# Performance work log

Measured on AMD Instinct MI355X. Metric: run time of the kernel, lower is better.

The kernel has to match this reference:

```python
import jax, jax.numpy as jnp
import numpy as np

N = 400_000      # total nodes
H = 256          # hidden_dim
G = 1024         # num_graphs (static; torch derives it from batch_idx.max()+1)
E1, E2, E3 = 7, 70, 300


def _linear_params(key, fan_in, fan_out):
    kw, kb = jax.random.split(key)
    bound = 1.0 / np.sqrt(fan_in)
    w = jax.random.uniform(kw, (fan_in, fan_out), jnp.float32, -bound, bound)
    b = jax.random.uniform(kb, (fan_out,), jnp.float32, -bound, bound)
    return w, b


def setup_inputs() -> dict:
    key = jax.random.key(0)
    ks = jax.random.split(key, 9)
    node_embeddings = jax.random.normal(ks[0], (N, H), jnp.float32)
    batch_idx = jnp.sort(jax.random.randint(ks[1], (N,), 0, G, jnp.int32))
    pool_w, pool_b = _linear_params(ks[2], H, H)
    ec1_w1, ec1_b1 = _linear_params(ks[3], H, H // 2)
    ec1_w2, ec1_b2 = _linear_params(ks[4], H // 2, E1)
    ec2_w1, ec2_b1 = _linear_params(ks[5], H + E1, H // 2)
    ec2_w2, ec2_b2 = _linear_params(ks[6], H // 2, E2)
    ec3_w1, ec3_b1 = _linear_params(ks[7], H + E1 + E2, H // 2)
    ec3_w2, ec3_b2 = _linear_params(ks[8], H // 2, E3)
    return {
        'node_embeddings': node_embeddings, 'batch_idx': batch_idx,
        'pool_w': pool_w, 'pool_b': pool_b,
        'ec1_w1': ec1_w1, 'ec1_b1': ec1_b1, 'ec1_w2': ec1_w2, 'ec1_b2': ec1_b2,
        'ec2_w1': ec2_w1, 'ec2_b1': ec2_b1, 'ec2_w2': ec2_w2, 'ec2_b2': ec2_b2,
        'ec3_w1': ec3_w1, 'ec3_b1': ec3_b1, 'ec3_w2': ec3_w2, 'ec3_b2': ec3_b2,
    }


def reference(node_embeddings, batch_idx,
              pool_w, pool_b,
              ec1_w1, ec1_b1, ec1_w2, ec1_b2,
              ec2_w1, ec2_b1, ec2_w2, ec2_b2,
              ec3_w1, ec3_b1, ec3_w2, ec3_b2):
    # segment mean pooling: replaces the python loop over graphs in torch
    sums = jax.ops.segment_sum(node_embeddings, batch_idx, num_segments=G)
    counts = jax.ops.segment_sum(jnp.ones((node_embeddings.shape[0],), jnp.float32),
                                 batch_idx, num_segments=G)
    global_feat = sums / jnp.maximum(counts, 1.0)[:, None]  # [G, H]

    gelu = lambda x: jax.nn.gelu(x, approximate=False)  # torch GELU default = exact erf
    g = gelu(global_feat @ pool_w + pool_b)  # dropout is identity in eval

    ec1_logits = gelu(g @ ec1_w1 + ec1_b1) @ ec1_w2 + ec1_b2           # [G, E1]
    ec1_probs = jax.nn.softmax(ec1_logits, axis=-1)

    x2 = jnp.concatenate([g, ec1_probs], axis=-1)                      # [G, H+E1]
    ec2_logits = gelu(x2 @ ec2_w1 + ec2_b1) @ ec2_w2 + ec2_b2          # [G, E2]
    ec2_probs = jax.nn.softmax(ec2_logits, axis=-1)

    x3 = jnp.concatenate([g, ec1_probs, ec2_probs], axis=-1)           # [G, H+E1+E2]
    ec3_logits = gelu(x3 @ ec3_w1 + ec3_b1) @ ec3_w2 + ec3_b2          # [G, E3]

    return (ec1_logits, ec2_logits, ec3_logits, ec1_probs, g)
```

## Files before the change

kernel.cpp:

```cpp
#include <hip/hip_runtime.h>
#include <hip/hip_bf16.h>
#include <math.h>

#define NN 400000
#define GG 1024
#define E1 7
#define E2 70
#define E3 300

#define OFF_L1 0
#define OFF_L2 7168
#define OFF_L3 78848
#define OFF_P1 386048
#define OFF_G  393216

typedef float f32x4 __attribute__((ext_vector_type(4)));

__device__ __forceinline__ float gelu_exact(float v) {
  return 0.5f * v * (1.0f + erff(v * 0.70710678118654752f));
}

__global__ __launch_bounds__(256) void fused_kernel(
    const float* __restrict__ emb, const int* __restrict__ bidx,
    const float* __restrict__ pool_w, const float* __restrict__ pool_b,
    const float* __restrict__ w11, const float* __restrict__ b11,
    const float* __restrict__ w12, const float* __restrict__ b12,
    const float* __restrict__ w21, const float* __restrict__ b21,
    const float* __restrict__ w22, const float* __restrict__ b22,
    const float* __restrict__ w31, const float* __restrict__ b31,
    const float* __restrict__ w32, const float* __restrict__ b32,
    float* __restrict__ out) {
  const int g0 = blockIdx.x * 2;
  const int tid = threadIdx.x;
  const int wave = tid >> 6, lane = tid & 63;

  __shared__ int seg[3];
  __shared__ float xs[2][336];
  __shared__ float hs[2][128];
  __shared__ float os[2][72];
  __shared__ f32x4 red[4][64];

  if (tid < 3) {
    const int target = g0 + tid;
    int lo = 0, hi = NN;
    while (lo < hi) {
      int mid = (lo + hi) >> 1;
      if (bidx[mid] < target) lo = mid + 1; else hi = mid;
    }
    seg[tid] = lo;
  }
  __syncthreads();

  for (int gg = 0; gg < 2; ++gg) {
    const int start = seg[gg], end = seg[gg + 1];
    const int hn = end - start;
    const int q0 = start + (hn * wave) / 4;
    const int q1 = start + (hn * (wave + 1)) / 4;
    const f32x4* __restrict__ p = (const f32x4*)emb + (size_t)q0 * 64 + lane;
    int n = q1 - q0;

    f32x4 a0 = {0.f, 0.f, 0.f, 0.f};
    f32x4 a1 = a0, a2 = a0, a3 = a0, a4 = a0, a5 = a0, a6 = a0, a7 = a0;
    for (; n >= 8; n -= 8, p += 512) {
      f32x4 v0 = __builtin_nontemporal_load(p + 0);
      f32x4 v1 = __builtin_nontemporal_load(p + 64);
      f32x4 v2 = __builtin_nontemporal_load(p + 128);
      f32x4 v3 = __builtin_nontemporal_load(p + 192);
      f32x4 v4 = __builtin_nontemporal_load(p + 256);
      f32x4 v5 = __builtin_nontemporal_load(p + 320);
      f32x4 v6 = __builtin_nontemporal_load(p + 384);
      f32x4 v7 = __builtin_nontemporal_load(p + 448);
      a0 += v0; a1 += v1; a2 += v2; a3 += v3;
      a4 += v4; a5 += v5; a6 += v6; a7 += v7;
    }
    for (; n > 0; --n, p += 64) {
      a0 += __builtin_nontemporal_load(p);
    }
    a0 += a1; a2 += a3; a4 += a5; a6 += a7;
    a0 += a2; a4 += a6;
    a0 += a4;

    red[wave][lane] = a0;
    __syncthreads();
    if (tid < 64) {
      f32x4 s = ((red[0][tid] + red[1][tid]) + (red[2][tid] + red[3][tid]));
      const float inv = 1.0f / (float)max(hn, 1);
      s *= inv;
      xs[gg][4 * tid + 0] = s.x;
      xs[gg][4 * tid + 1] = s.y;
      xs[gg][4 * tid + 2] = s.z;
      xs[gg][4 * tid + 3] = s.w;
    }
    __syncthreads();
  }

  {
    const int j = tid;
    float a0 = 0.f, a1 = 0.f;
#pragma unroll 8
    for (int k = 0; k < 256; ++k) {
      const float w = pool_w[k * 256 + j];
      a0 += xs[0][k] * w;
      a1 += xs[1][k] * w;
    }
    const float bj = pool_b[j];
    a0 = gelu_exact(a0 + bj);
    a1 = gelu_exact(a1 + bj);
    __syncthreads();
    xs[0][j] = a0;
    xs[1][j] = a1;
    out[OFF_G + (g0 + 0) * 256 + j] = a0;
    out[OFF_G + (g0 + 1) * 256 + j] = a1;
  }
  __syncthreads();

  {
    const int r = tid >> 7, j = tid & 127;
    float a = 0.f;
#pragma unroll 8
    for (int k = 0; k < 256; ++k) a += xs[r][k] * w11[k * 128 + j];
    hs[r][j] = gelu_exact(a + b11[j]);
  }
  __syncthreads();
  if (tid < 2 * E1) {
    const int r2 = tid / E1, j2 = tid - r2 * E1;
    float acc = b12[j2];
#pragma unroll 8
    for (int k = 0; k < 128; ++k) acc += hs[r2][k] * w12[k * E1 + j2];
    os[r2][j2] = acc;
    out[OFF_L1 + (g0 + r2) * E1 + j2] = acc;
  }
  __syncthreads();
  if (tid < 2) {
    float m = os[tid][0];
    for (int q = 1; q < E1; ++q) m = fmaxf(m, os[tid][q]);
    float s = 0.f;
    for (int q = 0; q < E1; ++q) { float e = expf(os[tid][q] - m); os[tid][q] = e; s += e; }
    const float inv = 1.0f / s;
    for (int q = 0; q < E1; ++q) os[tid][q] *= inv;
  }
  __syncthreads();
  if (tid < 2 * E1) {
    const int r2 = tid / E1, j2 = tid - r2 * E1;
    const float v = os[r2][j2];
    out[OFF_P1 + (g0 + r2) * E1 + j2] = v;
    xs[r2][256 + j2] = v;
  }
  __syncthreads();

  {
    const int r = tid >> 7, j = tid & 127;
    float a = 0.f;
#pragma unroll 8
    for (int k = 0; k < 256 + E1; ++k) a += xs[r][k] * w21[k * 128 + j];
    hs[r][j] = gelu_exact(a + b21[j]);
  }
  __syncthreads();
  if (tid < 2 * E2) {
    const int r2 = tid / E2, j2 = tid - r2 * E2;
    float acc = b22[j2];
#pragma unroll 8
    for (int k = 0; k < 128; ++k) acc += hs[r2][k] * w22[k * E2 + j2];
    os[r2][j2] = acc;
    out[OFF_L2 + (g0 + r2) * E2 + j2] = acc;
  }
  __syncthreads();
  if (tid < 2) {
    float m = os[tid][0];
    for (int q = 1; q < E2; ++q) m = fmaxf(m, os[tid][q]);
    float s = 0.f;
    for (int q = 0; q < E2; ++q) { float e = expf(os[tid][q] - m); os[tid][q] = e; s += e; }
    const float inv = 1.0f / s;
    for (int q = 0; q < E2; ++q) os[tid][q] *= inv;
  }
  __syncthreads();
  if (tid < 2 * E2) {
    const int r2 = tid / E2, j2 = tid - r2 * E2;
    xs[r2][256 + E1 + j2] = os[r2][j2];
  }
  __syncthreads();

  {
    const int r = tid >> 7, j = tid & 127;
    float a = 0.f;
#pragma unroll 8
    for (int k = 0; k < 256 + E1 + E2; ++k) a += xs[r][k] * w31[k * 128 + j];
    hs[r][j] = gelu_exact(a + b31[j]);
  }
  __syncthreads();
  for (int idx = tid; idx < 2 * E3; idx += 256) {
    const int r2 = idx / E3, j2 = idx - r2 * E3;
    float acc = b32[j2];
#pragma unroll 8
    for (int k = 0; k < 128; ++k) acc += hs[r2][k] * w32[k * E3 + j2];
    out[OFF_L3 + (g0 + r2) * E3 + j2] = acc;
  }
}

extern "C" void kernel_launch(void* const* d_in, const int* in_sizes, int n_in,
                              void* d_out, int out_size, void* d_ws, size_t ws_size,
                              hipStream_t stream) {
  const float* emb    = (const float*)d_in[0];
  const int*   bidx   = (const int*)d_in[1];
  const float* pool_w = (const float*)d_in[2];
  const float* pool_b = (const float*)d_in[3];
  const float* w11    = (const float*)d_in[4];
  const float* b11    = (const float*)d_in[5];
  const float* w12    = (const float*)d_in[6];
  const float* b12    = (const float*)d_in[7];
  const float* w21    = (const float*)d_in[8];
  const float* b21    = (const float*)d_in[9];
  const float* w22    = (const float*)d_in[10];
  const float* b22    = (const float*)d_in[11];
  const float* w31    = (const float*)d_in[12];
  const float* b31    = (const float*)d_in[13];
  const float* w32    = (const float*)d_in[14];
  const float* b32    = (const float*)d_in[15];
  float* out = (float*)d_out;

  fused_kernel<<<GG / 2, 256, 0, stream>>>(
      emb, bidx, pool_w, pool_b, w11, b11, w12, b12,
      w21, b21, w22, b22, w31, b31, w32, b32, out);
}
```

Measured before the change: 113.8 us.

## Process one graph per block and split hidden-layer K across thread halves

Launches one block per graph instead of two graphs per block, doubling the grid to 1024 blocks so more CUs stream the node embeddings concurrently. The hidden-layer matvecs now split the reduction dimension across the two 128-thread halves and combine partial sums in shared memory. The cost is that weight matrices are re-read from cache by twice as many blocks and there are extra barriers per layer.

```diff
diff --git a/kernel.cpp b/kernel.cpp
--- a/kernel.cpp
+++ b/kernel.cpp
@@ -30,18 +30,19 @@
     const float* __restrict__ w31, const float* __restrict__ b31,
     const float* __restrict__ w32, const float* __restrict__ b32,
     float* __restrict__ out) {
-  const int g0 = blockIdx.x * 2;
+  const int g = blockIdx.x;
   const int tid = threadIdx.x;
   const int wave = tid >> 6, lane = tid & 63;
 
-  __shared__ int seg[3];
-  __shared__ float xs[2][336];
-  __shared__ float hs[2][128];
-  __shared__ float os[2][72];
+  __shared__ int seg[2];
+  __shared__ float xs[336];
+  __shared__ float hs[128];
+  __shared__ float hpart[2][128];
+  __shared__ float os[72];
   __shared__ f32x4 red[4][64];
 
-  if (tid < 3) {
-    const int target = g0 + tid;
+  if (tid < 2) {
+    const int target = g + tid;
     int lo = 0, hi = NN;
     while (lo < hi) {
       int mid = (lo + hi) >> 1;
@@ -51,8 +52,8 @@
   }
   __syncthreads();
 
-  for (int gg = 0; gg < 2; ++gg) {
-    const int start = seg[gg], end = seg[gg + 1];
+  {
+    const int start = seg[0], end = seg[1];
     const int hn = end - start;
     const int q0 = start + (hn * wave) / 4;
     const int q1 = start + (hn * (wave + 1)) / 4;
@@ -86,114 +87,110 @@
       f32x4 s = ((red[0][tid] + red[1][tid]) + (red[2][tid] + red[3][tid]));
       const float inv = 1.0f / (float)max(hn, 1);
       s *= inv;
-      xs[gg][4 * tid + 0] = s.x;
-      xs[gg][4 * tid + 1] = s.y;
-      xs[gg][4 * tid + 2] = s.z;
-      xs[gg][4 * tid + 3] = s.w;
+      xs[4 * tid + 0] = s.x;
+      xs[4 * tid + 1] = s.y;
+      xs[4 * tid + 2] = s.z;
+      xs[4 * tid + 3] = s.w;
     }
     __syncthreads();
   }
 
   {
     const int j = tid;
-    float a0 = 0.f, a1 = 0.f;
-#pragma unroll 8
-    for (int k = 0; k < 256; ++k) {
-      const float w = pool_w[k * 256 + j];
-      a0 += xs[0][k] * w;
-      a1 += xs[1][k] * w;
-    }
-    const float bj = pool_b[j];
-    a0 = gelu_exact(a0 + bj);
-    a1 = gelu_exact(a1 + bj);
+    float a0 = 0.f;
+#pragma unroll 8
+    for (int k = 0; k < 256; ++k) a0 += xs[k] * pool_w[k * 256 + j];
+    a0 = gelu_exact(a0 + pool_b[j]);
     __syncthreads();
-    xs[0][j] = a0;
-    xs[1][j] = a1;
-    out[OFF_G + (g0 + 0) * 256 + j] = a0;
-    out[OFF_G + (g0 + 1) * 256 + j] = a1;
-  }
-  __syncthreads();
-
-  {
-    const int r = tid >> 7, j = tid & 127;
+    xs[j] = a0;
+    out[OFF_G + g * 256 + j] = a0;
+  }
+  __syncthreads();
+
+  {
+    const int half = tid >> 7, j = tid & 127;
+    const int k0 = half * 128, k1 = k0 + 128;
     float a = 0.f;
 #pragma unroll 8
-    for (int k = 0; k < 256; ++k) a += xs[r][k] * w11[k * 128 + j];
-    hs[r][j] = gelu_exact(a + b11[j]);
-  }
-  __syncthreads();
-  if (tid < 2 * E1) {
-    const int r2 = tid / E1, j2 = tid - r2 * E1;
-    float acc = b12[j2];
-#pragma unroll 8
-    for (int k = 0; k < 128; ++k) acc += hs[r2][k] * w12[k * E1 + j2];
-    os[r2][j2] = acc;
-    out[OFF_L1 + (g0 + r2) * E1 + j2] = acc;
-  }
-  __syncthreads();
-  if (tid < 2) {
-    float m = os[tid][0];
-    for (int q = 1; q < E1; ++q) m = fmaxf(m, os[tid][q]);
+    for (int k = k0; k < k1; ++k) a += xs[k] * w11[k * 128 + j];
+    hpart[half][j] = a;
+  }
+  __syncthreads();
+  if (tid < 128) hs[tid] = gelu_exact(hpart[0][tid] + hpart[1][tid] + b11[tid]);
+  __syncthreads();
+  if (tid < E1) {
+    float acc = b12[tid];
+#pragma unroll 8
+    for (int k = 0; k < 128; ++k) acc += hs[k] * w12[k * E1 + tid];
+    os[tid] = acc;
+    out[OFF_L1 + g * E1 + tid] = acc;
+  }
+  __syncthreads();
+  if (tid == 0) {
+    float m = os[0];
+    for (int q = 1; q < E1; ++q) m = fmaxf(m, os[q]);
     float s = 0.f;
-    for (int q = 0; q < E1; ++q) { float e = expf(os[tid][q] - m); os[tid][q] = e; s += e; }
+    for (int q = 0; q < E1; ++q) { float e = expf(os[q] - m); os[q] = e; s += e; }
     const float inv = 1.0f / s;
-    for (int q = 0; q < E1; ++q) os[tid][q] *= inv;
-  }
-  __syncthreads();
-  if (tid < 2 * E1) {
-    const int r2 = tid / E1, j2 = tid - r2 * E1;
-    const float v = os[r2][j2];
-    out[OFF_P1 + (g0 + r2) * E1 + j2] = v;
-    xs[r2][256 + j2] = v;
-  }
-  __syncthreads();
-
-  {
-    const int r = tid >> 7, j = tid & 127;
+    for (int q = 0; q < E1; ++q) os[q] *= inv;
+  }
+  __syncthreads();
+  if (tid < E1) {
+    const float v = os[tid];
+    out[OFF_P1 + g * E1 + tid] = v;
+    xs[256 + tid] = v;
+  }
+  __syncthreads();
+
+  {
+    const int K1 = 256 + E1;
+    const int half = tid >> 7, j = tid & 127;
+    const int k0 = (K1 * half) / 2, k1 = (K1 * (half + 1)) / 2;
     float a = 0.f;
 #pragma unroll 8
-    for (int k = 0; k < 256 + E1; ++k) a += xs[r][k] * w21[k * 128 + j];
-    hs[r][j] = gelu_exact(a + b21[j]);
-  }
-  __syncthreads();
-  if (tid < 2 * E2) {
-    const int r2 = tid / E2, j2 = tid - r2 * E2;
-    float acc = b22[j2];
-#pragma unroll 8
-    for (int k = 0; k < 128; ++k) acc += hs[r2][k] * w22[k * E2 + j2];
-    os[r2][j2] = acc;
-    out[OFF_L2 + (g0 + r2) * E2 + j2] = acc;
-  }
-  __syncthreads();
-  if (tid < 2) {
-    float m = os[tid][0];
-    for (int q = 1; q < E2; ++q) m = fmaxf(m, os[tid][q]);
+    for (int k = k0; k < k1; ++k) a += xs[k] * w21[k * 128 + j];
+    hpart[half][j] = a;
+  }
+  __syncthreads();
+  if (tid < 128) hs[tid] = gelu_exact(hpart[0][tid] + hpart[1][tid] + b21[tid]);
+  __syncthreads();
+  if (tid < E2) {
+    float acc = b22[tid];
+#pragma unroll 8
+    for (int k = 0; k < 128; ++k) acc += hs[k] * w22[k * E2 + tid];
+    os[tid] = acc;
+    out[OFF_L2 + g * E2 + tid] = acc;
+  }
+  __syncthreads();
+  if (tid == 0) {
+    float m = os[0];
+    for (int q = 1; q < E2; ++q) m = fmaxf(m, os[q]);
     float s = 0.f;
-    for (int q = 0; q < E2; ++q) { float e = expf(os[tid][q] - m); os[tid][q] = e; s += e; }
+    for (int q = 0; q < E2; ++q) { float e = expf(os[q] - m); os[q] = e; s += e; }
     const float inv = 1.0f / s;
-    for (int q = 0; q < E2; ++q) os[tid][q] *= inv;
-  }
-  __syncthreads();
-  if (tid < 2 * E2) {
-    const int r2 = tid / E2, j2 = tid - r2 * E2;
-    xs[r2][256 + E1 + j2] = os[r2][j2];
-  }
-  __syncthreads();
-
-  {
-    const int r = tid >> 7, j = tid & 127;
+    for (int q = 0; q < E2; ++q) os[q] *= inv;
+  }
+  __syncthreads();
+  if (tid < E2) xs[256 + E1 + tid] = os[tid];
+  __syncthreads();
+
+  {
+    const int K1 = 256 + E1 + E2;
+    const int half = tid >> 7, j = tid & 127;
+    const int k0 = (K1 * half) / 2, k1 = (K1 * (half + 1)) / 2;
     float a = 0.f;
 #pragma unroll 8
-    for (int k = 0; k < 256 + E1 + E2; ++k) a += xs[r][k] * w31[k * 128 + j];
-    hs[r][j] = gelu_exact(a + b31[j]);
-  }
-  __syncthreads();
-  for (int idx = tid; idx < 2 * E3; idx += 256) {
-    const int r2 = idx / E3, j2 = idx - r2 * E3;
-    float acc = b32[j2];
-#pragma unroll 8
-    for (int k = 0; k < 128; ++k) acc += hs[r2][k] * w32[k * E3 + j2];
-    out[OFF_L3 + (g0 + r2) * E3 + j2] = acc;
+    for (int k = k0; k < k1; ++k) a += xs[k] * w31[k * 128 + j];
+    hpart[half][j] = a;
+  }
+  __syncthreads();
+  if (tid < 128) hs[tid] = gelu_exact(hpart[0][tid] + hpart[1][tid] + b31[tid]);
+  __syncthreads();
+  for (int j = tid; j < E3; j += 256) {
+    float acc = b32[j];
+#pragma unroll 8
+    for (int k = 0; k < 128; ++k) acc += hs[k] * w32[k * E3 + j];
+    out[OFF_L3 + g * E3 + j] = acc;
   }
 }
 
@@ -218,7 +215,7 @@
   const float* b32    = (const float*)d_in[15];
   float* out = (float*)d_out;
 
-  fused_kernel<<<GG / 2, 256, 0, stream>>>(
+  fused_kernel<<<GG, 256, 0, stream>>>(
       emb, bidx, pool_w, pool_b, w11, b11, w12, b12,
       w21, b21, w22, b22, w31, b31, w32, b32, out);
 }
```

New measurement: 135.4 us. +19.0%, slower.

## Split segment-mean pooling and MLP head into separate kernels with 4-row batching

Applied to the files above, without the earlier changes.

The single fused kernel becomes two: a segment-mean pooling kernel that writes pooled features to workspace, and an MLP kernel that handles 4 graphs per 512-thread block. In the MLP kernel the K dimension is split across thread groups and the partial sums are reduced through shared memory. Each weight load is reused across 4 rows instead of 2, which halves total weight traffic from global or L2 and shortens the serial MLP tail after the bandwidth-bound pooling phase. In exchange it adds a second launch, a workspace round trip, and more barriers.

```diff
diff --git a/kernel.cpp b/kernel.cpp
--- a/kernel.cpp
+++ b/kernel.cpp
@@ -20,24 +20,14 @@
   return 0.5f * v * (1.0f + erff(v * 0.70710678118654752f));
 }
 
-__global__ __launch_bounds__(256) void fused_kernel(
+__global__ __launch_bounds__(256) void seg_mean_kernel(
     const float* __restrict__ emb, const int* __restrict__ bidx,
-    const float* __restrict__ pool_w, const float* __restrict__ pool_b,
-    const float* __restrict__ w11, const float* __restrict__ b11,
-    const float* __restrict__ w12, const float* __restrict__ b12,
-    const float* __restrict__ w21, const float* __restrict__ b21,
-    const float* __restrict__ w22, const float* __restrict__ b22,
-    const float* __restrict__ w31, const float* __restrict__ b31,
-    const float* __restrict__ w32, const float* __restrict__ b32,
-    float* __restrict__ out) {
+    float* __restrict__ gfm) {
   const int g0 = blockIdx.x * 2;
   const int tid = threadIdx.x;
   const int wave = tid >> 6, lane = tid & 63;
 
   __shared__ int seg[3];
-  __shared__ float xs[2][336];
-  __shared__ float hs[2][128];
-  __shared__ float os[2][72];
   __shared__ f32x4 red[4][64];
 
   if (tid < 3) {
@@ -86,114 +76,199 @@
       f32x4 s = ((red[0][tid] + red[1][tid]) + (red[2][tid] + red[3][tid]));
       const float inv = 1.0f / (float)max(hn, 1);
       s *= inv;
-      xs[gg][4 * tid + 0] = s.x;
-      xs[gg][4 * tid + 1] = s.y;
-      xs[gg][4 * tid + 2] = s.z;
-      xs[gg][4 * tid + 3] = s.w;
+      ((f32x4*)gfm)[(size_t)(g0 + gg) * 64 + tid] = s;
     }
     __syncthreads();
   }
-
-  {
-    const int j = tid;
-    float a0 = 0.f, a1 = 0.f;
-#pragma unroll 8
-    for (int k = 0; k < 256; ++k) {
+}
+
+#define RB 4
+
+__global__ __launch_bounds__(512) void mlp_kernel(
+    const float* __restrict__ gfm,
+    const float* __restrict__ pool_w, const float* __restrict__ pool_b,
+    const float* __restrict__ w11, const float* __restrict__ b11,
+    const float* __restrict__ w12, const float* __restrict__ b12,
+    const float* __restrict__ w21, const float* __restrict__ b21,
+    const float* __restrict__ w22, const float* __restrict__ b22,
+    const float* __restrict__ w31, const float* __restrict__ b31,
+    const float* __restrict__ w32, const float* __restrict__ b32,
+    float* __restrict__ out) {
+  const int r0 = blockIdx.x * RB;
+  const int t = threadIdx.x;
+
+  __shared__ float xs[RB][336];
+  __shared__ float sbuf[2048];
+  __shared__ float hs[RB][128];
+  __shared__ float os[RB][72];
+  __shared__ float lp[8][32];
+
+  for (int idx = t; idx < RB * 256; idx += 512) {
+    const int r = idx >> 8, j = idx & 255;
+    xs[r][j] = gfm[(size_t)(r0 + r) * 256 + j];
+  }
+  __syncthreads();
+
+  {
+    const int ks = t >> 8, j = t & 255;
+    const int k0 = ks * 128, k1 = k0 + 128;
+    float a0 = 0.f, a1 = 0.f, a2 = 0.f, a3 = 0.f;
+#pragma unroll 8
+    for (int k = k0; k < k1; ++k) {
       const float w = pool_w[k * 256 + j];
-      a0 += xs[0][k] * w;
-      a1 += xs[1][k] * w;
-    }
-    const float bj = pool_b[j];
-    a0 = gelu_exact(a0 + bj);
-    a1 = gelu_exact(a1 + bj);
-    __syncthreads();
-    xs[0][j] = a0;
-    xs[1][j] = a1;
-    out[OFF_G + (g0 + 0) * 256 + j] = a0;
-    out[OFF_G + (g0 + 1) * 256 + j] = a1;
-  }
-  __syncthreads();
-
-  {
-    const int r = tid >> 7, j = tid & 127;
-    float a = 0.f;
-#pragma unroll 8
-    for (int k = 0; k < 256; ++k) a += xs[r][k] * w11[k * 128 + j];
-    hs[r][j] = gelu_exact(a + b11[j]);
-  }
-  __syncthreads();
-  if (tid < 2 * E1) {
-    const int r2 = tid / E1, j2 = tid - r2 * E1;
-    float acc = b12[j2];
-#pragma unroll 8
-    for (int k = 0; k < 128; ++k) acc += hs[r2][k] * w12[k * E1 + j2];
-    os[r2][j2] = acc;
-    out[OFF_L1 + (g0 + r2) * E1 + j2] = acc;
-  }
-  __syncthreads();
-  if (tid < 2) {
-    float m = os[tid][0];
-    for (int q = 1; q < E1; ++q) m = fmaxf(m, os[tid][q]);
+      a0 += xs[0][k] * w; a1 += xs[1][k] * w;
+      a2 += xs[2][k] * w; a3 += xs[3][k] * w;
+    }
+    sbuf[ks * 1024 + 0 * 256 + j] = a0;
+    sbuf[ks * 1024 + 1 * 256 + j] = a1;
+    sbuf[ks * 1024 + 2 * 256 + j] = a2;
+    sbuf[ks * 1024 + 3 * 256 + j] = a3;
+  }
+  __syncthreads();
+  for (int idx = t; idx < RB * 256; idx += 512) {
+    const int r = idx >> 8, j = idx & 255;
+    const float v = gelu_exact(sbuf[r * 256 + j] + sbuf[1024 + r * 256 + j] + pool_b[j]);
+    xs[r][j] = v;
+    out[OFF_G + (size_t)(r0 + r) * 256 + j] = v;
+  }
+  __syncthreads();
+
+  {
+    const int ks = t >> 7, j = t & 127;
+    const int k0 = ks * 64, k1 = k0 + 64;
+    float a0 = 0.f, a1 = 0.f, a2 = 0.f, a3 = 0.f;
+#pragma unroll 8
+    for (int k = k0; k < k1; ++k) {
+      const float w = w11[k * 128 + j];
+      a0 += xs[0][k] * w; a1 += xs[1][k] * w;
+      a2 += xs[2][k] * w; a3 += xs[3][k] * w;
+    }
+    sbuf[ks * 512 + 0 * 128 + j] = a0;
+    sbuf[ks * 512 + 1 * 128 + j] = a1;
+    sbuf[ks * 512 + 2 * 128 + j] = a2;
+    sbuf[ks * 512 + 3 * 128 + j] = a3;
+  }
+  __syncthreads();
+  {
+    const int r = t >> 7, j = t & 127;
+    hs[r][j] = gelu_exact(sbuf[r * 128 + j] + sbuf[512 + r * 128 + j] +
+                          sbuf[1024 + r * 128 + j] + sbuf[1536 + r * 128 + j] + b11[j]);
+  }
+  __syncthreads();
+  if (t < 256) {
+    const int ks = t >> 5, sl = t & 31;
+    if (sl < RB * E1) {
+      const int r = sl / E1, j = sl - r * E1;
+      const int k0 = ks * 16, k1 = k0 + 16;
+      float a = 0.f;
+#pragma unroll 8
+      for (int k = k0; k < k1; ++k) a += hs[r][k] * w12[k * E1 + j];
+      lp[ks][sl] = a;
+    }
+  }
+  __syncthreads();
+  if (t < RB * E1) {
+    const int r = t / E1, j = t - r * E1;
+    float acc = b12[j];
+#pragma unroll
+    for (int ks = 0; ks < 8; ++ks) acc += lp[ks][t];
+    os[r][j] = acc;
+    out[OFF_L1 + (size_t)(r0 + r) * E1 + j] = acc;
+  }
+  __syncthreads();
+  if (t < RB) {
+    float m = os[t][0];
+    for (int q = 1; q < E1; ++q) m = fmaxf(m, os[t][q]);
     float s = 0.f;
-    for (int q = 0; q < E1; ++q) { float e = expf(os[tid][q] - m); os[tid][q] = e; s += e; }
+    for (int q = 0; q < E1; ++q) { float e = expf(os[t][q] - m); os[t][q] = e; s += e; }
     const float inv = 1.0f / s;
-    for (int q = 0; q < E1; ++q) os[tid][q] *= inv;
-  }
-  __syncthreads();
-  if (tid < 2 * E1) {
-    const int r2 = tid / E1, j2 = tid - r2 * E1;
-    const float v = os[r2][j2];
-    out[OFF_P1 + (g0 + r2) * E1 + j2] = v;
-    xs[r2][256 + j2] = v;
-  }
-  __syncthreads();
-
-  {
-    const int r = tid >> 7, j = tid & 127;
-    float a = 0.f;
-#pragma unroll 8
-    for (int k = 0; k < 256 + E1; ++k) a += xs[r][k] * w21[k * 128 + j];
-    hs[r][j] = gelu_exact(a + b21[j]);
-  }
-  __syncthreads();
-  if (tid < 2 * E2) {
-    const int r2 = tid / E2, j2 = tid - r2 * E2;
-    float acc = b22[j2];
-#pragma unroll 8
-    for (int k = 0; k < 128; ++k) acc += hs[r2][k] * w22[k * E2 + j2];
-    os[r2][j2] = acc;
-    out[OFF_L2 + (g0 + r2) * E2 + j2] = acc;
-  }
-  __syncthreads();
-  if (tid < 2) {
-    float m = os[tid][0];
-    for (int q = 1; q < E2; ++q) m = fmaxf(m, os[tid][q]);
+    for (int q = 0; q < E1; ++q) os[t][q] *= inv;
+  }
+  __syncthreads();
+  if (t < RB * E1) {
+    const int r = t / E1, j = t - r * E1;
+    const float v = os[r][j];
+    out[OFF_P1 + (size_t)(r0 + r) * E1 + j] = v;
+    xs[r][256 + j] = v;
+  }
+  __syncthreads();
+
+  {
+    const int K1 = 256 + E1;
+    const int ks = t >> 7, j = t & 127;
+    const int k0 = (K1 * ks) / 4, k1 = (K1 * (ks + 1)) / 4;
+    float a0 = 0.f, a1 = 0.f, a2 = 0.f, a3 = 0.f;
+#pragma unroll 8
+    for (int k = k0; k < k1; ++k) {
+      const float w = w21[k * 128 + j];
+      a0 += xs[0][k] * w; a1 += xs[1][k] * w;
+      a2 += xs[2][k] * w; a3 += xs[3][k] * w;
+    }
+    sbuf[ks * 512 + 0 * 128 + j] = a0;
+    sbuf[ks * 512 + 1 * 128 + j] = a1;
+    sbuf[ks * 512 + 2 * 128 + j] = a2;
+    sbuf[ks * 512 + 3 * 128 + j] = a3;
+  }
+  __syncthreads();
+  {
+    const int r = t >> 7, j = t & 127;
+    hs[r][j] = gelu_exact(sbuf[r * 128 + j] + sbuf[512 + r * 128 + j] +
+                          sbuf[1024 + r * 128 + j] + sbuf[1536 + r * 128 + j] + b21[j]);
+  }
+  __syncthreads();
+  if (t < RB * E2) {
+    const int r = t / E2, j = t - r * E2;
+    float acc = b22[j];
+#pragma unroll 8
+    for (int k = 0; k < 128; ++k) acc += hs[r][k] * w22[k * E2 + j];
+    os[r][j] = acc;
+    out[OFF_L2 + (size_t)(r0 + r) * E2 + j] = acc;
+  }
+  __syncthreads();
+  if (t < RB) {
+    float m = os[t][0];
+    for (int q = 1; q < E2; ++q) m = fmaxf(m, os[t][q]);
     float s = 0.f;
-    for (int q = 0; q < E2; ++q) { float e = expf(os[tid][q] - m); os[tid][q] = e; s += e; }
+    for (int q = 0; q < E2; ++q) { float e = expf(os[t][q] - m); os[t][q] = e; s += e; }
     const float inv = 1.0f / s;
-    for (int q = 0; q < E2; ++q) os[tid][q] *= inv;
-  }
-  __syncthreads();
-  if (tid < 2 * E2) {
-    const int r2 = tid / E2, j2 = tid - r2 * E2;
-    xs[r2][256 + E1 + j2] = os[r2][j2];
-  }
-  __syncthreads();
-
-  {
-    const int r = tid >> 7, j = tid & 127;
-    float a = 0.f;
-#pragma unroll 8
-    for (int k = 0; k < 256 + E1 + E2; ++k) a += xs[r][k] * w31[k * 128 + j];
-    hs[r][j] = gelu_exact(a + b31[j]);
-  }
-  __syncthreads();
-  for (int idx = tid; idx < 2 * E3; idx += 256) {
-    const int r2 = idx / E3, j2 = idx - r2 * E3;
-    float acc = b32[j2];
-#pragma unroll 8
-    for (int k = 0; k < 128; ++k) acc += hs[r2][k] * w32[k * E3 + j2];
-    out[OFF_L3 + (g0 + r2) * E3 + j2] = acc;
+    for (int q = 0; q < E2; ++q) os[t][q] *= inv;
+  }
+  __syncthreads();
+  if (t < RB * E2) {
+    const int r = t / E2, j = t - r * E2;
+    xs[r][256 + E1 + j] = os[r][j];
+  }
+  __syncthreads();
+
+  {
+    const int K1 = 256 + E1 + E2;
+    const int ks = t >> 7, j = t & 127;
+    const int k0 = (K1 * ks) / 4, k1 = (K1 * (ks + 1)) / 4;
+    float a0 = 0.f, a1 = 0.f, a2 = 0.f, a3 = 0.f;
+#pragma unroll 8
+    for (int k = k0; k < k1; ++k) {
+      const float w = w31[k * 128 + j];
+      a0 += xs[0][k] * w; a1 += xs[1][k] * w;
+      a2 += xs[2][k] * w; a3 += xs[3][k] * w;
+    }
+    sbuf[ks * 512 + 0 * 128 + j] = a0;
+    sbuf[ks * 512 + 1 * 128 + j] = a1;
+    sbuf[ks * 512 + 2 * 128 + j] = a2;
+    sbuf[ks * 512 + 3 * 128 + j] = a3;
+  }
+  __syncthreads();
+  {
+    const int r = t >> 7, j = t & 127;
+    hs[r][j] = gelu_exact(sbuf[r * 128 + j] + sbuf[512 + r * 128 + j] +
+                          sbuf[1024 + r * 128 + j] + sbuf[1536 + r * 128 + j] + b31[j]);
+  }
+  __syncthreads();
+  for (int idx = t; idx < RB * E3; idx += 512) {
+    const int r = idx / E3, j = idx - r * E3;
+    float acc = b32[j];
+#pragma unroll 8
+    for (int k = 0; k < 128; ++k) acc += hs[r][k] * w32[k * E3 + j];
+    out[OFF_L3 + (size_t)(r0 + r) * E3 + j] = acc;
   }
 }
 
@@ -217,8 +292,11 @@
   const float* w32    = (const float*)d_in[14];
   const float* b32    = (const float*)d_in[15];
   float* out = (float*)d_out;
-
-  fused_kernel<<<GG / 2, 256, 0, stream>>>(
-      emb, bidx, pool_w, pool_b, w11, b11, w12, b12,
-      w21, b21, w22, b22, w31, b31, w32, b32, out);
+  float* gfm = (float*)d_ws;
+
+  seg_mean_kernel<<<GG / 2, 256, 0, stream>>>(emb, bidx, gfm);
+  mlp_kernel<<<GG / RB, 512, 0, stream>>>(gfm, pool_w, pool_b,
+                                          w11, b11, w12, b12,
+                                          w21, b21, w22, b22,
+                                          w31, b31, w32, b32, out);
 }
```

Result: faster. 105.8 us, median of 2 (-7.0%).
